# Kernel optimization log

Measured on AMD Instinct MI355X. Metric: run time of the kernel, lower is better.

## Reference

```python
import jax, jax.numpy as jnp
import numpy as np

PATCH = 4
WINDOW = 4
MAX_ROUNDS = 4
MIN_ROUNDS = 2
LAMBDA_P = 0.2
TOPK = 8


def _ln(x, g, b, eps=1e-5):
    m = x.mean(-1, keepdims=True)
    v = ((x - m) ** 2).mean(-1, keepdims=True)
    return (x - m) / jnp.sqrt(v + eps) * g + b


def _mlp(x, w1, b1, w2, b2):
    # Linear -> exact GELU -> Linear (matches nn.GELU default)
    return jax.nn.gelu(x @ w1 + b1, approximate=False) @ w2 + b2


def setup_inputs() -> dict:
    key = jax.random.key(0)
    ks = jax.random.split(key, 24)
    B, T, D, V = 16, 4096, 256, 256
    s = 0.02
    w = lambda i, shape: jax.random.normal(ks[i], shape, jnp.float32) * s
    z = lambda *shape: jnp.zeros(shape, jnp.float32)
    o = lambda *shape: jnp.ones(shape, jnp.float32)
    return {
        'x': jax.random.randint(ks[0], (B, T), 0, V),
        'emb': w(1, (V, D)), 'pos': w(2, (PATCH, D)),
        'gru_wih': w(3, (D, 3 * D)), 'gru_whh': w(4, (D, 3 * D)),
        'gru_bih': z(3 * D), 'gru_bhh': z(3 * D),
        'ln_p_g': o(D), 'ln_p_b': z(D),
        'sum_w': w(5, (D, D)), 'sum_b': z(D),
        'msg_w1': w(6, (2 * D, D)), 'msg_b1': z(D), 'msg_w2': w(7, (D, D)), 'msg_b2': z(D),
        'upd_w1': w(8, (2 * D, D)), 'upd_b1': z(D), 'upd_w2': w(9, (D, D)), 'upd_b2': z(D),
        'halt_w': w(10, (D, 1)), 'halt_b': z(1),
        'ln_mp_g': o(D), 'ln_mp_b': z(D),
        'q_w': w(11, (D, D)), 'q_b': z(D),
        'k_w': w(12, (D, D)), 'k_b': z(D),
        'v_w': w(13, (D, D)), 'v_b': z(D),
        'o_w': w(14, (D, D)), 'o_b': z(D),
        'bc_w': w(15, (D, D)), 'bc_b': z(D),
        'ln_f_g': o(D), 'ln_f_b': z(D),
        'head_w': w(16, (D, V)),
    }


def reference(x, emb, pos, gru_wih, gru_whh, gru_bih, gru_bhh, ln_p_g, ln_p_b,
              sum_w, sum_b, msg_w1, msg_b1, msg_w2, msg_b2, upd_w1, upd_b1,
              upd_w2, upd_b2, halt_w, halt_b, ln_mp_g, ln_mp_b, q_w, q_b,
              k_w, k_b, v_w, v_b, o_w, o_b, bc_w, bc_b, ln_f_g, ln_f_b, head_w):
    B, T = x.shape
    D = emb.shape[1]
    Np = T // PATCH  # T is divisible by PATCH for these shapes (no pad needed)

    # --- GRU patch processor over B*Np sequences of length PATCH ---
    tok = x.reshape(B * Np, PATCH)
    hseq = emb[tok] + pos[None]  # [BN, P, D]

    def gru_step(h, xt):
        gi = xt @ gru_wih + gru_bih
        gh = h @ gru_whh + gru_bhh
        ir, iz, inn = jnp.split(gi, 3, -1)
        hr, hz, hn = jnp.split(gh, 3, -1)
        r = jax.nn.sigmoid(ir + hr)
        zz = jax.nn.sigmoid(iz + hz)
        n = jnp.tanh(inn + r * hn)
        h = (1 - zz) * n + zz * h
        return h, h

    h0 = jnp.zeros((B * Np, D), hseq.dtype)
    _, gout = jax.lax.scan(gru_step, h0, jnp.swapaxes(hseq, 0, 1))
    local = _ln(jnp.swapaxes(gout, 0, 1), ln_p_g, ln_p_b).reshape(B, Np, PATCH, D)
    summaries = local.mean(2) @ sum_w + sum_b  # [B, Np, D]

    # --- Local message passing with ACT-style halting (fixed MAX_ROUNDS) ---
    h = summaries
    remaining = jnp.ones((B, Np, 1), h.dtype)
    out_mp = jnp.zeros_like(h)
    kl = jnp.zeros((), h.dtype)
    for step in range(MAX_ROUNDS):
        padded = jnp.pad(h, ((0, 0), (WINDOW, 0), (0, 0)))
        # neighbors: self plus previous WINDOW patches -> [B, Np, W+1, D]
        neigh = jnp.stack([padded[:, WINDOW - w:WINDOW - w + Np] for w in range(WINDOW + 1)], axis=2)
        self_exp = jnp.broadcast_to(h[:, :, None, :], neigh.shape)
        msgs = _mlp(jnp.concatenate([self_exp, neigh], -1), msg_w1, msg_b1, msg_w2, msg_b2).mean(2)
        h = _ln(h + _mlp(jnp.concatenate([h, msgs], -1), upd_w1, upd_b1, upd_w2, upd_b2), ln_mp_g, ln_mp_b)
        if step < MIN_ROUNDS:
            hp = jnp.zeros((B, Np, 1), h.dtype)
        else:
            hp = jax.nn.sigmoid(h.mean(1, keepdims=True) @ halt_w + halt_b)  # [B,1,1]
            hp = jnp.broadcast_to(hp, (B, Np, 1))
        if step == MAX_ROUNDS - 1:
            hp = jnp.ones_like(hp)
        out_mp = out_mp + remaining * hp * h
        remaining = remaining * (1 - hp)
        p_geom = LAMBDA_P * (1 - LAMBDA_P) ** step
        # F.kl_div(log(mean+eps), log(p_geom), log_target=True) = p*(log p - log(mean+eps))
        kl = kl + p_geom * (np.log(p_geom) - jnp.log(hp.mean() + 1e-8))
    kl = kl / MAX_ROUNDS

    # --- Sparse top-k causal retrieval ---
    q = out_mp @ q_w + q_b
    kk = out_mp @ k_w + k_b
    v = out_mp @ v_w + v_b
    scores = jnp.einsum('bnd,bmd->bnm', q, kk) / np.sqrt(D).astype(np.float32)
    causal = jnp.tril(jnp.ones((Np, Np), bool))
    neg = jnp.asarray(-jnp.inf, scores.dtype)
    scores = jnp.where(causal[None], scores, neg)
    vals, idx = jax.lax.top_k(scores, TOPK)  # [B, Np, k]
    bi = jnp.arange(B)[:, None, None]
    ni = jnp.arange(Np)[None, :, None]
    sparse = jnp.full_like(scores, neg).at[bi, ni, idx].set(vals)
    attn = jax.nn.softmax(sparse, axis=-1)
    retrieved = jnp.einsum('bnm,bmd->bnd', attn, v) @ o_w + o_b

    # --- Broadcast back to tokens and project ---
    combined = out_mp + retrieved
    broad = combined @ bc_w + bc_b
    final = (local + broad[:, :, None, :]).reshape(B, Np * PATCH, D)[:, :T]
    logits = _ln(final, ln_f_g, ln_f_b) @ head_w
    return logits, kl
```

## Files before the change

### kernel.cpp

```cpp
#include <hip/hip_runtime.h>
#include <math.h>


typedef __bf16 bf16_t;
typedef bf16_t bf16x8 __attribute__((ext_vector_type(8)));
typedef bf16_t bf16x4 __attribute__((ext_vector_type(4)));
typedef float f32x4 __attribute__((ext_vector_type(4)));

#define GF_BIAS 1
#define GF_GELU 4
#define GF_RES 8
#define GF_F32OUT 32

__device__ __forceinline__ float gelu_exact(float x) {
  return 0.5f * x * (1.0f + erff(x * 0.7071067811865475f));
}

__device__ __forceinline__ float sigm(float x) { return 1.f / (1.f + expf(-x)); }

__device__ __forceinline__ float wave_sum(float v) {
#pragma unroll
  for (int o = 32; o; o >>= 1) v += __shfl_xor(v, o, 64);
  return v;
}

__device__ __forceinline__ void gload16(const void* g, void* l) {
  __builtin_amdgcn_global_load_lds(
      (const __attribute__((address_space(1))) void*)g,
      (__attribute__((address_space(3))) void*)l, 16, 0, 0);
}

__device__ __forceinline__ unsigned long long skey(float s, int m) {
  unsigned u = __float_as_uint(s);
  u ^= (u & 0x80000000u) ? 0xFFFFFFFFu : 0x80000000u;
  return ((unsigned long long)u << 32) | (unsigned)(0x7FFFFFFF - m);
}

template<int FLAGS>
__global__ __launch_bounds__(256)
void gemm_bt(const bf16_t* __restrict__ A, const bf16_t* __restrict__ Bt,
             void* __restrict__ Cv, const float* __restrict__ bias,
             const bf16_t* __restrict__ res,
             int lda, int ldb, int ldc, int ldr)
{
  __shared__ __align__(16) bf16_t As[128][64];
  __shared__ __align__(16) bf16_t Bs[128][64];
  const int m0 = blockIdx.x * 128, n0 = blockIdx.y * 128;
  const int tid = threadIdx.x, lane = tid & 63, wave = tid >> 6;
  const int wm = (wave >> 1) << 6, wn = (wave & 1) << 6;
  const int lr = lane & 15, lg = lane >> 4;
  const int cx = lane & 7;

  const int srow = wave * 32 + (lane >> 3);
  const int scol = (((lane & 7) ^ ((lane >> 3) & 7)) * 8);
  const bf16_t* ga = A  + (long long)(m0 + srow) * lda + scol;
  const bf16_t* gb = Bt + (long long)(n0 + srow) * ldb + scol;
  char* lA = (char*)(&As[srow][0]) + (lane & 7) * 16;
  char* lB = (char*)(&Bs[srow][0]) + (lane & 7) * 16;

  f32x4 acc[4][4] = {};

#pragma unroll
  for (int kt = 0; kt < 4; kt++) {
    const int ko = kt * 64;
#pragma unroll
    for (int q = 0; q < 4; q++) {
      gload16(ga + (long long)q * 8 * lda + ko, lA + q * 1024);
      gload16(gb + (long long)q * 8 * ldb + ko, lB + q * 1024);
    }
    __syncthreads();
#pragma unroll
    for (int kk = 0; kk < 2; kk++) {
      const int co = ((kk * 4 + lg) ^ cx) << 4;
      bf16x8 af[4], bfv[4];
#pragma unroll
      for (int i = 0; i < 4; i++)
        af[i]  = *(const bf16x8*)((char*)As + (wm + i * 16 + lr) * 128 + co);
#pragma unroll
      for (int j = 0; j < 4; j++)
        bfv[j] = *(const bf16x8*)((char*)Bs + (wn + j * 16 + lr) * 128 + co);
#pragma unroll
      for (int i = 0; i < 4; i++)
#pragma unroll
        for (int j = 0; j < 4; j++)
          acc[i][j] = __builtin_amdgcn_mfma_f32_16x16x32_bf16(af[i], bfv[j], acc[i][j], 0, 0, 0);
    }
    if (kt < 3) __syncthreads();
  }

#pragma unroll
  for (int i = 0; i < 4; i++) {
#pragma unroll
    for (int j = 0; j < 4; j++) {
      const int col = n0 + wn + j * 16 + lr;
      const float bval = (FLAGS & GF_BIAS) ? bias[col] : 0.f;
#pragma unroll
      for (int e = 0; e < 4; e++) {
        const int row = m0 + wm + i * 16 + lg * 4 + e;
        float v = acc[i][j][e] + bval;
        if (FLAGS & GF_RES) v += (float)res[(long long)row * ldr + col];
        if (FLAGS & GF_GELU) v = gelu_exact(v);
        const long long ci = (long long)row * ldc + col;
        if (FLAGS & GF_F32OUT) ((float*)Cv)[ci] = v;
        else                   ((bf16_t*)Cv)[ci] = (bf16_t)v;
      }
    }
  }
}

template<int FLAGS>
__global__ __launch_bounds__(256)
void gemm64(const bf16_t* __restrict__ A, const bf16_t* __restrict__ Bt,
            void* __restrict__ Cv, const float* __restrict__ bias,
            const bf16_t* __restrict__ res,
            int lda, int ldb, int ldc, int ldr)
{
  __shared__ __align__(16) bf16_t As[64][64];
  __shared__ __align__(16) bf16_t Bs[64][64];
  const int m0 = blockIdx.x * 64, n0 = blockIdx.y * 64;
  const int tid = threadIdx.x, lane = tid & 63, wave = tid >> 6;
  const int wm = (wave >> 1) * 32, wn = (wave & 1) * 32;
  const int lr = lane & 15, lg = lane >> 4;
  const int cx = lane & 7;

  const int srow = tid >> 3;
  const int scol = (((tid & 7) ^ (srow & 7)) * 8);
  const bf16_t* ga = A  + (long long)(m0 + srow) * lda + scol;
  const bf16_t* gb = Bt + (long long)(n0 + srow) * ldb + scol;
  char* lA = (char*)As + tid * 16;
  char* lB = (char*)Bs + tid * 16;

  f32x4 acc[2][2] = {};

#pragma unroll
  for (int kt = 0; kt < 4; kt++) {
    const int ko = kt * 64;
    gload16(ga + ko, lA);
    gload16(ga + 32LL * lda + ko, lA + 4096);
    gload16(gb + ko, lB);
    gload16(gb + 32LL * ldb + ko, lB + 4096);
    __syncthreads();
#pragma unroll
    for (int kk = 0; kk < 2; kk++) {
      const int co = ((kk * 4 + lg) ^ cx) << 4;
      bf16x8 af[2], bfv[2];
#pragma unroll
      for (int i = 0; i < 2; i++)
        af[i]  = *(const bf16x8*)((char*)As + (wm + i * 16 + lr) * 128 + co);
#pragma unroll
      for (int j = 0; j < 2; j++)
        bfv[j] = *(const bf16x8*)((char*)Bs + (wn + j * 16 + lr) * 128 + co);
#pragma unroll
      for (int i = 0; i < 2; i++)
#pragma unroll
        for (int j = 0; j < 2; j++)
          acc[i][j] = __builtin_amdgcn_mfma_f32_16x16x32_bf16(af[i], bfv[j], acc[i][j], 0, 0, 0);
    }
    if (kt < 3) __syncthreads();
  }

#pragma unroll
  for (int i = 0; i < 2; i++) {
#pragma unroll
    for (int j = 0; j < 2; j++) {
      const int col = n0 + wn + j * 16 + lr;
      const float bval = (FLAGS & GF_BIAS) ? bias[col] : 0.f;
#pragma unroll
      for (int e = 0; e < 4; e++) {
        const int row = m0 + wm + i * 16 + lg * 4 + e;
        float v = acc[i][j][e] + bval;
        if (FLAGS & GF_RES) v += (float)res[(long long)row * ldr + col];
        if (FLAGS & GF_GELU) v = gelu_exact(v);
        const long long ci = (long long)row * ldc + col;
        if (FLAGS & GF_F32OUT) ((float*)Cv)[ci] = v;
        else                   ((bf16_t*)Cv)[ci] = (bf16_t)v;
      }
    }
  }
}

template<int MODE>
__global__ __launch_bounds__(256)
void gemm_ln(const bf16_t* __restrict__ A, const bf16_t* __restrict__ Bt,
             bf16_t* __restrict__ C, const float* __restrict__ bias,
             const float* __restrict__ g, const float* __restrict__ bvec,
             bf16_t* __restrict__ OUTMP, const float* __restrict__ HP)
{
  __shared__ __align__(16) bf16_t As[64][64];
  __shared__ __align__(16) bf16_t Bs[256][64];
  __shared__ float redsum[4][64];
  __shared__ float redsq[4][64];
  const int m0 = blockIdx.x * 64;
  const int tid = threadIdx.x, lane = tid & 63, w = tid >> 6;
  const int lr = lane & 15, lg = lane >> 4, cx = lane & 7;

  f32x4 acc[4][4] = {};

#pragma unroll
  for (int kt = 0; kt < 4; kt++) {
    const int ko = kt * 64;
    {
      int cid = tid, r = cid >> 3, c = cid & 7;
      gload16(A + (long long)(m0 + r) * 256 + ko + ((c ^ (r & 7)) * 8), (char*)As + cid * 16);
      cid = tid + 256; r = cid >> 3; c = cid & 7;
      gload16(A + (long long)(m0 + r) * 256 + ko + ((c ^ (r & 7)) * 8), (char*)As + cid * 16);
    }
#pragma unroll
    for (int it = 0; it < 8; it++) {
      const int cid = it * 256 + tid, r = cid >> 3, c = cid & 7;
      gload16(Bt + (long long)r * 256 + ko + ((c ^ (r & 7)) * 8), (char*)Bs + cid * 16);
    }
    __syncthreads();
#pragma unroll
    for (int kk = 0; kk < 2; kk++) {
      const int co = ((kk * 4 + lg) ^ cx) << 4;
      bf16x8 af[4], bfv[4];
#pragma unroll
      for (int i = 0; i < 4; i++)
        af[i]  = *(const bf16x8*)((char*)As + (i * 16 + lr) * 128 + co);
#pragma unroll
      for (int j = 0; j < 4; j++)
        bfv[j] = *(const bf16x8*)((char*)Bs + (w * 64 + j * 16 + lr) * 128 + co);
#pragma unroll
      for (int i = 0; i < 4; i++)
#pragma unroll
        for (int j = 0; j < 4; j++)
          acc[i][j] = __builtin_amdgcn_mfma_f32_16x16x32_bf16(af[i], bfv[j], acc[i][j], 0, 0, 0);
    }
    if (kt < 3) __syncthreads();
  }

  float v[4][4][4];
  float rs[4][4], rq[4][4];
#pragma unroll
  for (int i = 0; i < 4; i++) {
#pragma unroll
    for (int e = 0; e < 4; e++) { rs[i][e] = 0.f; rq[i][e] = 0.f; }
  }
#pragma unroll
  for (int i = 0; i < 4; i++) {
#pragma unroll
    for (int j = 0; j < 4; j++) {
      const int col = w * 64 + j * 16 + lr;
      const float bval = bias[col];
#pragma unroll
      for (int e = 0; e < 4; e++) {
        const long long rg = m0 + i * 16 + lg * 4 + e;
        const float val = acc[i][j][e] + bval + (float)C[rg * 256 + col];
        v[i][j][e] = val;
        rs[i][e] += val;
        rq[i][e] += val * val;
      }
    }
  }
#pragma unroll
  for (int off = 1; off < 16; off <<= 1) {
#pragma unroll
    for (int i = 0; i < 4; i++)
#pragma unroll
      for (int e = 0; e < 4; e++) {
        rs[i][e] += __shfl_xor(rs[i][e], off, 64);
        rq[i][e] += __shfl_xor(rq[i][e], off, 64);
      }
  }
  if (lr == 0) {
#pragma unroll
    for (int i = 0; i < 4; i++)
#pragma unroll
      for (int e = 0; e < 4; e++) {
        redsum[w][i * 16 + lg * 4 + e] = rs[i][e];
        redsq[w][i * 16 + lg * 4 + e]  = rq[i][e];
      }
  }
  __syncthreads();
  float mean[4][4], rstd[4][4];
#pragma unroll
  for (int i = 0; i < 4; i++) {
#pragma unroll
    for (int e = 0; e < 4; e++) {
      const int r = i * 16 + lg * 4 + e;
      const float S = redsum[0][r] + redsum[1][r] + redsum[2][r] + redsum[3][r];
      const float Q = redsq[0][r] + redsq[1][r] + redsq[2][r] + redsq[3][r];
      const float m = S * (1.f / 256.f);
      float var = Q * (1.f / 256.f) - m * m;
      if (var < 0.f) var = 0.f;
      mean[i][e] = m;
      rstd[i][e] = rsqrtf(var + 1e-5f);
    }
  }
#pragma unroll
  for (int i = 0; i < 4; i++) {
#pragma unroll
    for (int j = 0; j < 4; j++) {
      const int col = w * 64 + j * 16 + lr;
      const float gg = g[col], bb = bvec[col];
#pragma unroll
      for (int e = 0; e < 4; e++) {
        const long long rg = m0 + i * 16 + lg * 4 + e;
        const float y = (v[i][j][e] - mean[i][e]) * rstd[i][e] * gg + bb;
        if (MODE == 0) {
          C[rg * 256 + col] = (bf16_t)y;
        } else {
          const float rem = 1.f - HP[(int)(rg >> 10)];
          OUTMP[rg * 256 + col] = (bf16_t)((float)OUTMP[rg * 256 + col] + rem * y);
        }
      }
    }
  }
}

__global__ __launch_bounds__(256)
void k_fatopk(const bf16_t* __restrict__ QKV, bf16_t* __restrict__ O) {
  __shared__ unsigned long long cand[4][16][8];
  __shared__ float wrow[16][8];
  __shared__ int   irow[16][8];
  const int b = blockIdx.y;
  const int qw = (int)((blockIdx.x + ((unsigned)(b * 21) & 63u)) & 63u);
  const int tid = threadIdx.x;
  const int wid = tid >> 6;
  const int lane = tid & 63;
  const int lr = lane & 15, lg = lane >> 4;
  const bf16_t* Qp = QKV + (long long)b * (1024LL * 768);
  const bf16_t* Kp = Qp + 256;
  const bf16_t* Vp = Qp + 512;
  const int q0 = qw * 16;
  const int qrow = q0 + lr;

  bf16x8 bq[8];
#pragma unroll
  for (int s = 0; s < 8; s++)
    bq[s] = *(const bf16x8*)(Qp + (long long)qrow * 768 + s * 32 + lg * 8);

  unsigned long long kv[8] = {0ull, 0ull, 0ull, 0ull, 0ull, 0ull, 0ull, 0ull};

#define INS8(KEY) {                                                     \
    const unsigned long long k_ = (KEY);                                \
    if (k_ > kv[7]) {                                                   \
      kv[7] = k_;                                                       \
      _Pragma("unroll")                                                 \
      for (int j_ = 7; j_ > 0; j_--)                                    \
        if (kv[j_] > kv[j_-1]) {                                        \
          const unsigned long long t_ = kv[j_];                         \
          kv[j_] = kv[j_-1]; kv[j_-1] = t_;                             \
        }                                                               \
    }                                                                   \
  }

  const int klim = qw + 1;
  for (int base = wid * 2; base < klim; base += 8) {
    const bool hasB = (base + 1 < klim);
    const int ktB = hasB ? base + 1 : base;
    const bf16_t* ka = Kp + (long long)(base * 16 + lr) * 768 + lg * 8;
    const bf16_t* kb = Kp + (long long)(ktB * 16 + lr) * 768 + lg * 8;
    bf16x8 afA[8], afB[8];
#pragma unroll
    for (int s = 0; s < 8; s++) afA[s] = *(const bf16x8*)(ka + s * 32);
#pragma unroll
    for (int s = 0; s < 8; s++) afB[s] = *(const bf16x8*)(kb + s * 32);
    f32x4 a0 = {}, a1 = {}, b0 = {}, b1 = {};
    __builtin_amdgcn_s_setprio(1);
#pragma unroll
    for (int s = 0; s < 8; s += 2) {
      a0 = __builtin_amdgcn_mfma_f32_16x16x32_bf16(afA[s],     bq[s],     a0, 0, 0, 0);
      a1 = __builtin_amdgcn_mfma_f32_16x16x32_bf16(afA[s + 1], bq[s + 1], a1, 0, 0, 0);
      b0 = __builtin_amdgcn_mfma_f32_16x16x32_bf16(afB[s],     bq[s],     b0, 0, 0, 0);
      b1 = __builtin_amdgcn_mfma_f32_16x16x32_bf16(afB[s + 1], bq[s + 1], b1, 0, 0, 0);
    }
    __builtin_amdgcn_s_setprio(0);
#pragma unroll
    for (int e = 0; e < 4; e++) {
      const int m = base * 16 + lg * 4 + e;
      if (m <= qrow) INS8(skey((a0[e] + a1[e]) * 0.0625f, m));
    }
    if (hasB) {
#pragma unroll
      for (int e = 0; e < 4; e++) {
        const int m = ktB * 16 + lg * 4 + e;
        if (m <= qrow) INS8(skey((b0[e] + b1[e]) * 0.0625f, m));
      }
    }
  }
#undef INS8

#pragma unroll
  for (int r = 0; r < 8; r++) {
    unsigned long long mk = kv[0];
    unsigned long long ok = __shfl_xor(mk, 16, 64); if (ok > mk) mk = ok;
    ok = __shfl_xor(mk, 32, 64); if (ok > mk) mk = ok;
    if (lg == 0) cand[wid][lr][r] = mk;
    if (kv[0] == mk && mk != 0ull) {
#pragma unroll
      for (int j = 0; j < 7; j++) kv[j] = kv[j + 1];
      kv[7] = 0ull;
    }
  }
  __syncthreads();

  if (wid == 0) {
    unsigned long long kv2[8];
#pragma unroll
    for (int j = 0; j < 8; j++) kv2[j] = cand[lg][lr][j];
    float wv[8]; int wi[8];
#pragma unroll
    for (int r = 0; r < 8; r++) {
      unsigned long long mk = kv2[0];
      unsigned long long ok = __shfl_xor(mk, 16, 64); if (ok > mk) mk = ok;
      ok = __shfl_xor(mk, 32, 64); if (ok > mk) mk = ok;
      if (mk != 0ull) {
        unsigned hi = (unsigned)(mk >> 32);
        hi ^= (hi & 0x80000000u) ? 0x80000000u : 0xFFFFFFFFu;
        wv[r] = __uint_as_float(hi);
        wi[r] = 0x7FFFFFFF - (int)(unsigned)(mk & 0xFFFFFFFFu);
      } else {
        wv[r] = 0.f; wi[r] = -1;
      }
      if (kv2[0] == mk && mk != 0ull) {
#pragma unroll
        for (int j = 0; j < 7; j++) kv2[j] = kv2[j + 1];
        kv2[7] = 0ull;
      }
    }
    const float mx = wv[0];
    float w8[8]; float den = 0.f;
#pragma unroll
    for (int j = 0; j < 8; j++) {
      w8[j] = (wi[j] >= 0) ? expf(wv[j] - mx) : 0.f;
      den += w8[j];
    }
    const float inv = 1.f / den;
    if (lg == 0) {
#pragma unroll
      for (int j = 0; j < 8; j++) {
        wrow[lr][j] = w8[j] * inv;
        irow[lr][j] = wi[j];
      }
    }
  }
  __syncthreads();

  const int rr = wid * 4 + lg;
  const int c0 = (lane & 15) * 16;
  f32x4 av[4] = {};
#pragma unroll
  for (int j = 0; j < 8; j++) {
    const int idx = irow[rr][j];
    if (idx >= 0) {
      const float wj = wrow[rr][j];
      const bf16_t* vr = Vp + (long long)idx * 768 + c0;
      const bf16x8 v0 = *(const bf16x8*)vr;
      const bf16x8 v1 = *(const bf16x8*)(vr + 8);
#pragma unroll
      for (int e = 0; e < 4; e++) {
        av[0][e] = fmaf(wj, (float)v0[e],     av[0][e]);
        av[1][e] = fmaf(wj, (float)v0[4 + e], av[1][e]);
        av[2][e] = fmaf(wj, (float)v1[e],     av[2][e]);
        av[3][e] = fmaf(wj, (float)v1[4 + e], av[3][e]);
      }
    }
  }
  bf16_t* op = O + ((long long)b * 1024 + q0 + rr) * 256 + c0;
  bf16x8 o0, o1;
#pragma unroll
  for (int e = 0; e < 4; e++) {
    o0[e] = (bf16_t)av[0][e]; o0[4 + e] = (bf16_t)av[1][e];
    o1[e] = (bf16_t)av[2][e]; o1[4 + e] = (bf16_t)av[3][e];
  }
  *(bf16x8*)op = o0;
  *(bf16x8*)(op + 8) = o1;
}

struct TD { const float* src; bf16_t* dst; int N; int k0; int ld; };
struct PrepArgs {
  TD d[16];
  const float* emb; const float* pos; bf16_t* XE;
  const float* msg_b1; const float* msg_b2; const float* upd_w1; const float* upd_b1;
  const float* q_b; const float* k_b; const float* v_b;
  float* BIAS3; float* QKVB;
};

__global__ __launch_bounds__(256) void k_prep(PrepArgs pa) {
  const int y = blockIdx.y, x = blockIdx.x, d = threadIdx.x;
  if (y < 16) {
    TD t = pa.d[y];
    if (x >= t.N) return;
    if (t.k0 < 0) t.dst[(long long)x * 256 + d] = (bf16_t)t.src[(long long)x * t.ld + d];
    else          t.dst[(long long)x * 256 + d] = (bf16_t)t.src[(long long)(t.k0 + d) * t.ld + x];
  } else if (y == 16) {
    const int p = x >> 8, v = x & 255;
    pa.XE[(long long)x * 256 + d] = (bf16_t)(pa.emb[v * 256 + d] + pa.pos[p * 256 + d]);
  } else {
    if      (x == 0) pa.BIAS3[d] = pa.msg_b1[d];
    else if (x == 1) pa.BIAS3[256 + d] = 0.f;
    else if (x == 2) {
      float acc = pa.upd_b1[d];
      for (int k = 0; k < 256; k++) acc += pa.msg_b2[k] * pa.upd_w1[(long long)(256 + k) * 256 + d];
      pa.BIAS3[512 + d] = acc;
    }
    else if (x == 3) pa.QKVB[d] = pa.q_b[d];
    else if (x == 4) pa.QKVB[256 + d] = pa.k_b[d];
    else if (x == 5) pa.QKVB[512 + d] = pa.v_b[d];
  }
}

__global__ __launch_bounds__(256)
void k_gru_gate(const int* __restrict__ x, const bf16_t* __restrict__ gitab,
                const bf16_t* __restrict__ GH, const float* __restrict__ bhh,
                bf16_t* __restrict__ H, bf16_t* __restrict__ LOC, int t)
{
  const int s = blockIdx.x * 4 + (threadIdx.x >> 6);
  const int lane = threadIdx.x & 63, d0 = lane * 4;
  const int v = x[s * 4 + t];
  const bf16_t* gi = gitab + (long long)(t * 256 + v) * 768;
  const bf16x4 g_r = *(const bf16x4*)(gi + d0);
  const bf16x4 g_z = *(const bf16x4*)(gi + 256 + d0);
  const bf16x4 g_n = *(const bf16x4*)(gi + 512 + d0);
  float hr[4], hz[4], hn[4], hp[4];
  if (t == 0) {
#pragma unroll
    for (int e = 0; e < 4; e++) {
      hr[e] = bhh[d0 + e]; hz[e] = bhh[256 + d0 + e]; hn[e] = bhh[512 + d0 + e];
      hp[e] = 0.f;
    }
  } else {
    const bf16_t* gh = GH + (long long)s * 768;
    const bf16x4 a = *(const bf16x4*)(gh + d0);
    const bf16x4 b4 = *(const bf16x4*)(gh + 256 + d0);
    const bf16x4 c4 = *(const bf16x4*)(gh + 512 + d0);
    const bf16x4 hv = *(const bf16x4*)(H + (long long)s * 256 + d0);
#pragma unroll
    for (int e = 0; e < 4; e++) { hr[e] = a[e]; hz[e] = b4[e]; hn[e] = c4[e]; hp[e] = hv[e]; }
  }
  bf16x4 ho;
#pragma unroll
  for (int e = 0; e < 4; e++) {
    const float r = sigm((float)g_r[e] + hr[e]);
    const float zz = sigm((float)g_z[e] + hz[e]);
    const float nn = tanhf((float)g_n[e] + r * hn[e]);
    ho[e] = (bf16_t)((1.f - zz) * nn + zz * hp[e]);
  }
  *(bf16x4*)(H + (long long)s * 256 + d0) = ho;
  *(bf16x4*)(LOC + ((long long)s * 4 + t) * 256 + d0) = ho;
}

__global__ __launch_bounds__(256)
void k_ln(const bf16_t* __restrict__ X, const bf16_t* __restrict__ ADD, int addmode,
          bf16_t* __restrict__ OUT, const float* __restrict__ g,
          const float* __restrict__ b)
{
  const long long r = (long long)blockIdx.x * 4 + (threadIdx.x >> 6);
  const int d0 = (threadIdx.x & 63) * 4;
  const bf16x4 xv = *(const bf16x4*)(X + r * 256 + d0);
  float xf[4];
#pragma unroll
  for (int e = 0; e < 4; e++) xf[e] = (float)xv[e];
  if (addmode == 1) {
    const bf16x4 av = *(const bf16x4*)(ADD + r * 256 + d0);
#pragma unroll
    for (int e = 0; e < 4; e++) xf[e] += (float)av[e];
  } else if (addmode == 2) {
    const bf16x4 av = *(const bf16x4*)(ADD + (r >> 2) * 256 + d0);
#pragma unroll
    for (int e = 0; e < 4; e++) xf[e] += (float)av[e];
  }
  const float mean = wave_sum(xf[0] + xf[1] + xf[2] + xf[3]) * (1.f / 256.f);
  float q = 0.f;
#pragma unroll
  for (int e = 0; e < 4; e++) { const float dx = xf[e] - mean; q += dx * dx; }
  const float rstd = rsqrtf(wave_sum(q) * (1.f / 256.f) + 1e-5f);
  const float4 gv = *(const float4*)(g + d0);
  const float4 bv = *(const float4*)(b + d0);
  const float gg[4] = {gv.x, gv.y, gv.z, gv.w};
  const float bb[4] = {bv.x, bv.y, bv.z, bv.w};
  bf16x4 ov;
#pragma unroll
  for (int e = 0; e < 4; e++) ov[e] = (bf16_t)((xf[e] - mean) * rstd * gg[e] + bb[e]);
  *(bf16x4*)(OUT + r * 256 + d0) = ov;
}

__global__ __launch_bounds__(256)
void k_lnp4(bf16_t* __restrict__ LOC, bf16_t* __restrict__ SUMB,
            const float* __restrict__ g, const float* __restrict__ b)
{
  const long long s = (long long)blockIdx.x * 4 + (threadIdx.x >> 6);
  const int d0 = (threadIdx.x & 63) * 4;
  const float4 gv = *(const float4*)(g + d0);
  const float4 bv = *(const float4*)(b + d0);
  const float gg[4] = {gv.x, gv.y, gv.z, gv.w};
  const float bb[4] = {bv.x, bv.y, bv.z, bv.w};
  float accd[4] = {0.f, 0.f, 0.f, 0.f};
#pragma unroll
  for (int t = 0; t < 4; t++) {
    bf16_t* row = LOC + (s * 4 + t) * 256 + d0;
    const bf16x4 xv = *(const bf16x4*)row;
    float xf[4];
#pragma unroll
    for (int e = 0; e < 4; e++) xf[e] = (float)xv[e];
    const float mean = wave_sum(xf[0] + xf[1] + xf[2] + xf[3]) * (1.f / 256.f);
    float q = 0.f;
#pragma unroll
    for (int e = 0; e < 4; e++) { const float dx = xf[e] - mean; q += dx * dx; }
    const float rstd = rsqrtf(wave_sum(q) * (1.f / 256.f) + 1e-5f);
    bf16x4 ov;
#pragma unroll
    for (int e = 0; e < 4; e++) {
      const float y = (xf[e] - mean) * rstd * gg[e] + bb[e];
      ov[e] = (bf16_t)y;
      accd[e] += y;
    }
    *(bf16x4*)row = ov;
  }
  bf16x4 sv;
#pragma unroll
  for (int e = 0; e < 4; e++) sv[e] = (bf16_t)(accd[e] * 0.25f);
  *(bf16x4*)(SUMB + s * 256 + d0) = sv;
}

__global__ __launch_bounds__(256)
void k_gelumix(const bf16_t* __restrict__ A3, bf16_t* __restrict__ G)
{
  const long long s = (long long)blockIdx.x * 4 + (threadIdx.x >> 6);
  const int n = (int)(s & 1023);
  const int d0 = (threadIdx.x & 63) * 4;
  const bf16x4 av = *(const bf16x4*)(A3 + s * 768 + d0);
  float a[4];
#pragma unroll
  for (int e = 0; e < 4; e++) a[e] = (float)av[e];
  float acc[4] = {0.f, 0.f, 0.f, 0.f};
  const bf16_t* bbase = A3 + s * 768 + 256 + d0;
#pragma unroll
  for (int w = 0; w <= 4; w++) {
    if (n >= w) {
      const bf16x4 bn = *(const bf16x4*)(bbase - (long long)w * 768);
#pragma unroll
      for (int e = 0; e < 4; e++) acc[e] += gelu_exact(a[e] + (float)bn[e]);
    } else {
#pragma unroll
      for (int e = 0; e < 4; e++) acc[e] += gelu_exact(a[e]);
    }
  }
  bf16x4 ov;
#pragma unroll
  for (int e = 0; e < 4; e++) ov[e] = (bf16_t)(acc[e] * 0.2f);
  *(bf16x4*)(G + s * 256 + d0) = ov;
}

__global__ __launch_bounds__(64)
void k_halt1(const bf16_t* __restrict__ Hm, float* __restrict__ PS) {
  const int c = blockIdx.x, b = blockIdx.y, d0 = threadIdx.x * 4;
  float acc[4] = {0.f, 0.f, 0.f, 0.f};
  const bf16_t* base = Hm + ((long long)b * 1024 + c * 32) * 256 + d0;
#pragma unroll 4
  for (int n = 0; n < 32; n++) {
    const bf16x4 hv = *(const bf16x4*)(base + (long long)n * 256);
#pragma unroll
    for (int e = 0; e < 4; e++) acc[e] += (float)hv[e];
  }
  float4 o4; o4.x = acc[0]; o4.y = acc[1]; o4.z = acc[2]; o4.w = acc[3];
  *(float4*)(PS + ((long long)b * 32 + c) * 256 + d0) = o4;
}

__global__ __launch_bounds__(1024)
void k_halt2kl(const float* __restrict__ PS, const float* __restrict__ hw,
               const float* __restrict__ hb, float* __restrict__ HP,
               float* __restrict__ out) {
  __shared__ float sh[16];
  const int b = threadIdx.x >> 6, lane = threadIdx.x & 63, d0 = lane * 4;
  float acc[4] = {0.f, 0.f, 0.f, 0.f};
  for (int c = 0; c < 32; c++) {
    const float4 p4 = *(const float4*)(PS + ((long long)b * 32 + c) * 256 + d0);
    acc[0] += p4.x; acc[1] += p4.y; acc[2] += p4.z; acc[3] += p4.w;
  }
  const float4 w4 = *(const float4*)(hw + d0);
  float val = (acc[0] * w4.x + acc[1] * w4.y + acc[2] * w4.z + acc[3] * w4.w) * (1.f / 1024.f);
  val = wave_sum(val);
  if (lane == 0) {
    const float hp = sigm(val + hb[0]);
    HP[b] = hp;
    sh[b] = hp;
  }
  __syncthreads();
  if (threadIdx.x == 0) {
    float s = 0.f;
    for (int bb = 0; bb < 16; bb++) s += sh[bb];
    const float hpm = s * (1.f / 16.f);
    const float l8 = logf(1e-8f);
    const float p0 = 0.2f, p1 = 0.16f, p2 = 0.128f, p3 = 0.1024f;
    const float kl = p0 * (logf(p0) - l8)
                   + p1 * (logf(p1) - l8)
                   + p2 * (logf(p2) - logf(hpm + 1e-8f))
                   + p3 * (logf(p3) - logf(1.f + 1e-8f));
    out[0] = kl * 0.25f;
  }
}

__global__ __launch_bounds__(256)
void k_outmp(const bf16_t* __restrict__ Hm, const float* __restrict__ HP,
             bf16_t* __restrict__ O) {
  const long long s = (long long)blockIdx.x * 4 + (threadIdx.x >> 6);
  const int d0 = (threadIdx.x & 63) * 4;
  const int b = (int)(s >> 10);
  const float hp = HP[b];
  const bf16x4 hv = *(const bf16x4*)(Hm + s * 256 + d0);
  bf16x4 ov;
#pragma unroll
  for (int e = 0; e < 4; e++) ov[e] = (bf16_t)(hp * (float)hv[e]);
  *(bf16x4*)(O + s * 256 + d0) = ov;
}

extern "C" void kernel_launch(void* const* d_in, const int* in_sizes, int n_in,
                              void* d_out, int out_size, void* d_ws, size_t ws_size,
                              hipStream_t stream) {
  (void)in_sizes; (void)n_in; (void)ws_size;
  const int*   x      = (const int*)d_in[0];
  const float* emb    = (const float*)d_in[1];
  const float* pos    = (const float*)d_in[2];
  const float* wih    = (const float*)d_in[3];
  const float* whh    = (const float*)d_in[4];
  const float* bih    = (const float*)d_in[5];
  const float* bhh    = (const float*)d_in[6];
  const float* lnp_g  = (const float*)d_in[7];
  const float* lnp_b  = (const float*)d_in[8];
  const float* sum_w  = (const float*)d_in[9];
  const float* sum_b  = (const float*)d_in[10];
  const float* msg_w1 = (const float*)d_in[11];
  const float* msg_b1 = (const float*)d_in[12];
  const float* msg_w2 = (const float*)d_in[13];
  const float* msg_b2 = (const float*)d_in[14];
  const float* upd_w1 = (const float*)d_in[15];
  const float* upd_b1 = (const float*)d_in[16];
  const float* upd_w2 = (const float*)d_in[17];
  const float* upd_b2 = (const float*)d_in[18];
  const float* halt_w = (const float*)d_in[19];
  const float* halt_b = (const float*)d_in[20];
  const float* lnm_g  = (const float*)d_in[21];
  const float* lnm_b  = (const float*)d_in[22];
  const float* q_b    = (const float*)d_in[24];
  const float* k_b    = (const float*)d_in[26];
  const float* v_b    = (const float*)d_in[28];
  const float* o_b    = (const float*)d_in[30];
  const float* bc_b   = (const float*)d_in[32];
  const float* lnf_g  = (const float*)d_in[33];
  const float* lnf_b  = (const float*)d_in[34];

  char* base = (char*)d_ws;
  size_t off = 0;
  auto alloc = [&](size_t bytes) -> void* {
    void* p = (void*)(base + off);
    off += (bytes + 255) & ~(size_t)255;
    return p;
  };
  const size_t SL2 = 16384ull * 256 * 2;
  bf16_t* WIHT  = (bf16_t*)alloc(768 * 256 * 2);
  bf16_t* WHHT  = (bf16_t*)alloc(768 * 256 * 2);
  bf16_t* SUMT  = (bf16_t*)alloc(256 * 256 * 2);
  bf16_t* MW    = (bf16_t*)alloc(768 * 256 * 2);
  bf16_t* W2T   = (bf16_t*)alloc(256 * 256 * 2);
  bf16_t* W2NT  = (bf16_t*)alloc(256 * 256 * 2);
  bf16_t* UW1MT = (bf16_t*)alloc(256 * 256 * 2);
  bf16_t* UW2T  = (bf16_t*)alloc(256 * 256 * 2);
  bf16_t* WCB   = (bf16_t*)alloc(256 * 256 * 2);
  bf16_t* QKVW  = (bf16_t*)alloc(768 * 256 * 2);
  bf16_t* OT    = (bf16_t*)alloc(256 * 256 * 2);
  bf16_t* BCT   = (bf16_t*)alloc(256 * 256 * 2);
  bf16_t* HEADT = (bf16_t*)alloc(256 * 256 * 2);
  float*  BIAS3 = (float*)alloc(768 * 4);
  float*  QKVB  = (float*)alloc(768 * 4);
  bf16_t* XE    = (bf16_t*)alloc(1024ull * 256 * 2);
  bf16_t* GITAB = (bf16_t*)alloc(1024ull * 768 * 2);
  bf16_t* LOCb  = (bf16_t*)alloc(65536ull * 256 * 2);

  char*   SCR   = (char*)alloc(16ull * 1024 * 1024 * 4);
  bf16_t* GH    = (bf16_t*)SCR;
  bf16_t* H     = (bf16_t*)(SCR + 25165824);
  bf16_t* SUMB  = (bf16_t*)(SCR + 33554432);
  bf16_t* A3    = (bf16_t*)(SCR + 41943040);

  bf16_t* HMP   = (bf16_t*)alloc(SL2);
  bf16_t* G     = (bf16_t*)alloc(SL2);
  bf16_t* BROAD = (bf16_t*)alloc(SL2);
  bf16_t* UB    = (bf16_t*)alloc(SL2);
  bf16_t* U2B   = (bf16_t*)alloc(SL2);
  bf16_t* OUTMP = (bf16_t*)alloc(SL2);
  bf16_t* QKV   = (bf16_t*)alloc(16384ull * 768 * 2);
  float*  PS    = (float*)alloc(512ull * 256 * 4);
  float*  HP    = (float*)alloc(64);
  bf16_t* ATT   = UB;
  bf16_t* COMB  = U2B;
  float*  out   = (float*)d_out;
  float*  klout = out + (out_size - 1);

  PrepArgs pa;
  pa.d[0]  = { wih,                    WIHT,            768, 0,   768 };
  pa.d[1]  = { whh,                    WHHT,            768, 0,   768 };
  pa.d[2]  = { sum_w,                  SUMT,            256, 0,   256 };
  pa.d[3]  = { msg_w1,                 MW,              256, 0,   256 };
  pa.d[4]  = { msg_w1,                 MW + 256 * 256,  256, 256, 256 };
  pa.d[5]  = { upd_w1,                 MW + 512 * 256,  256, 0,   256 };
  pa.d[6]  = { msg_w2,                 W2T,             256, 0,   256 };
  pa.d[7]  = { upd_w1,                 UW1MT,           256, 256, 256 };
  pa.d[8]  = { upd_w2,                 UW2T,            256, 0,   256 };
  pa.d[9]  = { (const float*)d_in[23], QKVW,            256, 0,   256 };
  pa.d[10] = { (const float*)d_in[25], QKVW + 256*256,  256, 0,   256 };
  pa.d[11] = { (const float*)d_in[27], QKVW + 512*256,  256, 0,   256 };
  pa.d[12] = { (const float*)d_in[29], OT,              256, 0,   256 };
  pa.d[13] = { (const float*)d_in[31], BCT,             256, 0,   256 };
  pa.d[14] = { (const float*)d_in[35], HEADT,           256, 0,   256 };
  pa.d[15] = { msg_w2,                 W2NT,            256, -1,  256 };
  pa.emb = emb; pa.pos = pos; pa.XE = XE;
  pa.msg_b1 = msg_b1; pa.msg_b2 = msg_b2; pa.upd_w1 = upd_w1; pa.upd_b1 = upd_b1;
  pa.q_b = q_b; pa.k_b = k_b; pa.v_b = v_b;
  pa.BIAS3 = BIAS3; pa.QKVB = QKVB;
  k_prep<<<dim3(1024, 18), 256, 0, stream>>>(pa);

  gemm64<0><<<dim3(4, 4), 256, 0, stream>>>(
      UW1MT, W2NT, WCB, nullptr, nullptr, 256, 256, 256, 0);

  gemm64<GF_BIAS><<<dim3(16, 12), 256, 0, stream>>>(
      XE, WIHT, GITAB, bih, nullptr, 256, 256, 768, 0);

  k_gru_gate<<<4096, 256, 0, stream>>>(x, GITAB, GH, bhh, H, LOCb, 0);
  for (int t = 1; t < 4; t++) {
    gemm_bt<GF_BIAS><<<dim3(128, 6), 256, 0, stream>>>(
        H, WHHT, GH, bhh, nullptr, 256, 256, 768, 0);
    k_gru_gate<<<4096, 256, 0, stream>>>(x, GITAB, GH, bhh, H, LOCb, t);
  }

  k_lnp4<<<4096, 256, 0, stream>>>(LOCb, SUMB, lnp_g, lnp_b);
  gemm64<GF_BIAS><<<dim3(256, 4), 256, 0, stream>>>(
      SUMB, SUMT, HMP, sum_b, nullptr, 256, 256, 256, 0);

  for (int step = 0; step < 4; step++) {
    gemm_bt<GF_BIAS><<<dim3(128, 6), 256, 0, stream>>>(
        HMP, MW, A3, BIAS3, nullptr, 256, 256, 768, 0);
    k_gelumix<<<4096, 256, 0, stream>>>(A3, G);
    gemm64<GF_RES | GF_GELU><<<dim3(256, 4), 256, 0, stream>>>(
        G, WCB, UB, nullptr, A3 + 512, 256, 256, 256, 768);
    if (step == 3) {
      gemm_ln<1><<<256, 256, 0, stream>>>(
          UB, UW2T, HMP, upd_b2, lnm_g, lnm_b, OUTMP, HP);
    } else {
      gemm_ln<0><<<256, 256, 0, stream>>>(
          UB, UW2T, HMP, upd_b2, lnm_g, lnm_b, nullptr, nullptr);
      if (step == 2) {
        k_halt1<<<dim3(32, 16), 64, 0, stream>>>(HMP, PS);
        k_halt2kl<<<1, 1024, 0, stream>>>(PS, halt_w, halt_b, HP, klout);
        k_outmp<<<4096, 256, 0, stream>>>(HMP, HP, OUTMP);
      }
    }
  }

  gemm_bt<GF_BIAS><<<dim3(128, 6), 256, 0, stream>>>(
      OUTMP, QKVW, QKV, QKVB, nullptr, 256, 256, 768, 0);
  k_fatopk<<<dim3(64, 16), 256, 0, stream>>>(QKV, ATT);
  gemm64<GF_BIAS | GF_RES><<<dim3(256, 4), 256, 0, stream>>>(
      ATT, OT, COMB, o_b, OUTMP, 256, 256, 256, 256);
  gemm64<GF_BIAS><<<dim3(256, 4), 256, 0, stream>>>(
      COMB, BCT, BROAD, bc_b, nullptr, 256, 256, 256, 0);

  k_ln<<<16384, 256, 0, stream>>>(LOCb, BROAD, 2, LOCb, lnf_g, lnf_b);
  gemm_bt<GF_F32OUT><<<dim3(512, 2), 256, 0, stream>>>(
      LOCb, HEADT, out, nullptr, nullptr, 256, 256, 256, 0);
}
```

Before: 466.7 us.

## Split top-k retrieval into key-split scan and separate merge/gather kernel

The fused top-k attention kernel is split in two. A scan kernel spreads each query tile's causal key range over four blocks, with each wave keeping partial top-8 lists that are written to a global candidate buffer in the scratch region. A second kernel merges the 16 partial lists per query row with wave shuffles, computes softmax weights and gathers the V rows. This gives the scan more parallelism and better balance across the triangular causal workload, at the cost of an extra launch and a global round trip for the candidates.

```diff
diff --git a/kernel.cpp b/kernel.cpp
--- a/kernel.cpp
+++ b/kernel.cpp
@@ -310,19 +310,15 @@
 }
 
 __global__ __launch_bounds__(256)
-void k_fatopk(const bf16_t* __restrict__ QKV, bf16_t* __restrict__ O) {
-  __shared__ unsigned long long cand[4][16][8];
-  __shared__ float wrow[16][8];
-  __shared__ int   irow[16][8];
-  const int b = blockIdx.y;
+void k_fascan(const bf16_t* __restrict__ QKV,
+              unsigned long long* __restrict__ CAND) {
+  const int b = blockIdx.z;
+  const int ks = blockIdx.y;
   const int qw = (int)((blockIdx.x + ((unsigned)(b * 21) & 63u)) & 63u);
-  const int tid = threadIdx.x;
-  const int wid = tid >> 6;
-  const int lane = tid & 63;
+  const int tid = threadIdx.x, wid = tid >> 6, lane = tid & 63;
   const int lr = lane & 15, lg = lane >> 4;
   const bf16_t* Qp = QKV + (long long)b * (1024LL * 768);
   const bf16_t* Kp = Qp + 256;
-  const bf16_t* Vp = Qp + 512;
   const int q0 = qw * 16;
   const int qrow = q0 + lr;
 
@@ -346,127 +342,94 @@
     }                                                                   \
   }
 
-  const int klim = qw + 1;
-  for (int base = wid * 2; base < klim; base += 8) {
-    const bool hasB = (base + 1 < klim);
-    const int ktB = hasB ? base + 1 : base;
-    const bf16_t* ka = Kp + (long long)(base * 16 + lr) * 768 + lg * 8;
-    const bf16_t* kb = Kp + (long long)(ktB * 16 + lr) * 768 + lg * 8;
-    bf16x8 afA[8], afB[8];
-#pragma unroll
-    for (int s = 0; s < 8; s++) afA[s] = *(const bf16x8*)(ka + s * 32);
-#pragma unroll
-    for (int s = 0; s < 8; s++) afB[s] = *(const bf16x8*)(kb + s * 32);
-    f32x4 a0 = {}, a1 = {}, b0 = {}, b1 = {};
+  for (int kt = ks + 4 * wid; kt <= qw; kt += 16) {
+    const bf16_t* ka = Kp + (long long)(kt * 16 + lr) * 768 + lg * 8;
+    bf16x8 af[8];
+#pragma unroll
+    for (int s = 0; s < 8; s++) af[s] = *(const bf16x8*)(ka + s * 32);
+    f32x4 a0 = {}, a1 = {};
     __builtin_amdgcn_s_setprio(1);
 #pragma unroll
     for (int s = 0; s < 8; s += 2) {
-      a0 = __builtin_amdgcn_mfma_f32_16x16x32_bf16(afA[s],     bq[s],     a0, 0, 0, 0);
-      a1 = __builtin_amdgcn_mfma_f32_16x16x32_bf16(afA[s + 1], bq[s + 1], a1, 0, 0, 0);
-      b0 = __builtin_amdgcn_mfma_f32_16x16x32_bf16(afB[s],     bq[s],     b0, 0, 0, 0);
-      b1 = __builtin_amdgcn_mfma_f32_16x16x32_bf16(afB[s + 1], bq[s + 1], b1, 0, 0, 0);
+      a0 = __builtin_amdgcn_mfma_f32_16x16x32_bf16(af[s],     bq[s],     a0, 0, 0, 0);
+      a1 = __builtin_amdgcn_mfma_f32_16x16x32_bf16(af[s + 1], bq[s + 1], a1, 0, 0, 0);
     }
     __builtin_amdgcn_s_setprio(0);
 #pragma unroll
     for (int e = 0; e < 4; e++) {
-      const int m = base * 16 + lg * 4 + e;
+      const int m = kt * 16 + lg * 4 + e;
       if (m <= qrow) INS8(skey((a0[e] + a1[e]) * 0.0625f, m));
     }
-    if (hasB) {
-#pragma unroll
-      for (int e = 0; e < 4; e++) {
-        const int m = ktB * 16 + lg * 4 + e;
-        if (m <= qrow) INS8(skey((b0[e] + b1[e]) * 0.0625f, m));
-      }
-    }
   }
 #undef INS8
 
+  unsigned long long* cp =
+      CAND + (((long long)(b * 1024 + qrow)) * 16 + (ks * 4 + wid)) * 8;
 #pragma unroll
   for (int r = 0; r < 8; r++) {
     unsigned long long mk = kv[0];
     unsigned long long ok = __shfl_xor(mk, 16, 64); if (ok > mk) mk = ok;
     ok = __shfl_xor(mk, 32, 64); if (ok > mk) mk = ok;
-    if (lg == 0) cand[wid][lr][r] = mk;
+    if (lg == 0) cp[r] = mk;
     if (kv[0] == mk && mk != 0ull) {
 #pragma unroll
       for (int j = 0; j < 7; j++) kv[j] = kv[j + 1];
       kv[7] = 0ull;
     }
   }
-  __syncthreads();
-
-  if (wid == 0) {
-    unsigned long long kv2[8];
-#pragma unroll
-    for (int j = 0; j < 8; j++) kv2[j] = cand[lg][lr][j];
-    float wv[8]; int wi[8];
-#pragma unroll
-    for (int r = 0; r < 8; r++) {
-      unsigned long long mk = kv2[0];
-      unsigned long long ok = __shfl_xor(mk, 16, 64); if (ok > mk) mk = ok;
-      ok = __shfl_xor(mk, 32, 64); if (ok > mk) mk = ok;
-      if (mk != 0ull) {
-        unsigned hi = (unsigned)(mk >> 32);
-        hi ^= (hi & 0x80000000u) ? 0x80000000u : 0xFFFFFFFFu;
-        wv[r] = __uint_as_float(hi);
-        wi[r] = 0x7FFFFFFF - (int)(unsigned)(mk & 0xFFFFFFFFu);
-      } else {
-        wv[r] = 0.f; wi[r] = -1;
-      }
-      if (kv2[0] == mk && mk != 0ull) {
-#pragma unroll
-        for (int j = 0; j < 7; j++) kv2[j] = kv2[j + 1];
-        kv2[7] = 0ull;
-      }
-    }
-    const float mx = wv[0];
-    float w8[8]; float den = 0.f;
-#pragma unroll
-    for (int j = 0; j < 8; j++) {
-      w8[j] = (wi[j] >= 0) ? expf(wv[j] - mx) : 0.f;
-      den += w8[j];
-    }
-    const float inv = 1.f / den;
-    if (lg == 0) {
-#pragma unroll
-      for (int j = 0; j < 8; j++) {
-        wrow[lr][j] = w8[j] * inv;
-        irow[lr][j] = wi[j];
-      }
-    }
-  }
-  __syncthreads();
-
-  const int rr = wid * 4 + lg;
-  const int c0 = (lane & 15) * 16;
-  f32x4 av[4] = {};
+}
+
+__global__ __launch_bounds__(256)
+void k_sel8(const unsigned long long* __restrict__ CAND,
+            const bf16_t* __restrict__ QKV, bf16_t* __restrict__ O) {
+  const int n = blockIdx.x * 4 + (threadIdx.x >> 6);
+  const int b = blockIdx.y;
+  const int lane = threadIdx.x & 63;
+  const unsigned long long* base = CAND + ((long long)(b * 1024 + n)) * 128;
+  unsigned long long v0 = base[lane], v1 = base[lane + 64];
+  if (v1 > v0) { const unsigned long long t = v0; v0 = v1; v1 = t; }
+  float wv[8]; int wi[8];
+#pragma unroll
+  for (int r = 0; r < 8; r++) {
+    unsigned long long mk = v0;
+#pragma unroll
+    for (int off = 32; off; off >>= 1) {
+      const unsigned long long ok = __shfl_xor(mk, off, 64);
+      if (ok > mk) mk = ok;
+    }
+    if (mk != 0ull) {
+      unsigned hi = (unsigned)(mk >> 32);
+      hi ^= (hi & 0x80000000u) ? 0x80000000u : 0xFFFFFFFFu;
+      wv[r] = __uint_as_float(hi);
+      wi[r] = 0x7FFFFFFF - (int)(unsigned)(mk & 0xFFFFFFFFu);
+    } else {
+      wv[r] = 0.f; wi[r] = -1;
+    }
+    if (v0 == mk && mk != 0ull) { v0 = v1; v1 = 0ull; }
+  }
+  const float mx = wv[0];
+  float w8[8]; float den = 0.f;
 #pragma unroll
   for (int j = 0; j < 8; j++) {
-    const int idx = irow[rr][j];
-    if (idx >= 0) {
-      const float wj = wrow[rr][j];
-      const bf16_t* vr = Vp + (long long)idx * 768 + c0;
-      const bf16x8 v0 = *(const bf16x8*)vr;
-      const bf16x8 v1 = *(const bf16x8*)(vr + 8);
-#pragma unroll
-      for (int e = 0; e < 4; e++) {
-        av[0][e] = fmaf(wj, (float)v0[e],     av[0][e]);
-        av[1][e] = fmaf(wj, (float)v0[4 + e], av[1][e]);
-        av[2][e] = fmaf(wj, (float)v1[e],     av[2][e]);
-        av[3][e] = fmaf(wj, (float)v1[4 + e], av[3][e]);
-      }
-    }
-  }
-  bf16_t* op = O + ((long long)b * 1024 + q0 + rr) * 256 + c0;
-  bf16x8 o0, o1;
-#pragma unroll
-  for (int e = 0; e < 4; e++) {
-    o0[e] = (bf16_t)av[0][e]; o0[4 + e] = (bf16_t)av[1][e];
-    o1[e] = (bf16_t)av[2][e]; o1[4 + e] = (bf16_t)av[3][e];
-  }
-  *(bf16x8*)op = o0;
-  *(bf16x8*)(op + 8) = o1;
+    w8[j] = (wi[j] >= 0) ? expf(wv[j] - mx) : 0.f;
+    den += w8[j];
+  }
+  const float inv = 1.f / den;
+  const bf16_t* Vp = QKV + (long long)b * (1024LL * 768) + 512;
+  f32x4 av = {};
+#pragma unroll
+  for (int j = 0; j < 8; j++) {
+    if (wi[j] >= 0) {
+      const float wj = w8[j] * inv;
+      const bf16x4 vv = *(const bf16x4*)(Vp + (long long)wi[j] * 768 + lane * 4);
+#pragma unroll
+      for (int e = 0; e < 4; e++) av[e] = fmaf(wj, (float)vv[e], av[e]);
+    }
+  }
+  bf16x4 o4;
+#pragma unroll
+  for (int e = 0; e < 4; e++) o4[e] = (bf16_t)av[e];
+  *(bf16x4*)(O + ((long long)(b * 1024 + n)) * 256 + lane * 4) = o4;
 }
 
 struct TD { const float* src; bf16_t* dst; int N; int k0; int ld; };
@@ -774,6 +737,7 @@
   bf16_t* H     = (bf16_t*)(SCR + 25165824);
   bf16_t* SUMB  = (bf16_t*)(SCR + 33554432);
   bf16_t* A3    = (bf16_t*)(SCR + 41943040);
+  unsigned long long* CAND = (unsigned long long*)SCR;
 
   bf16_t* HMP   = (bf16_t*)alloc(SL2);
   bf16_t* G     = (bf16_t*)alloc(SL2);
@@ -851,7 +815,8 @@
 
   gemm_bt<GF_BIAS><<<dim3(128, 6), 256, 0, stream>>>(
       OUTMP, QKVW, QKV, QKVB, nullptr, 256, 256, 768, 0);
-  k_fatopk<<<dim3(64, 16), 256, 0, stream>>>(QKV, ATT);
+  k_fascan<<<dim3(64, 4, 16), 256, 0, stream>>>(QKV, CAND);
+  k_sel8<<<dim3(256, 16), 256, 0, stream>>>(CAND, QKV, ATT);
   gemm64<GF_BIAS | GF_RES><<<dim3(256, 4), 256, 0, stream>>>(
       ATT, OT, COMB, o_b, OUTMP, 256, 256, 256, 256);
   gemm64<GF_BIAS><<<dim3(256, 4), 256, 0, stream>>>(
```

New measurement: 492.0 us. +5.4%, slower.
